# Kernel tuning notes

Hardware: AMD Instinct MI355X
Metric: run time of the kernel (lower is better)

The kernel has to match this reference:

```python
import jax, jax.numpy as jnp
import numpy as np

BLOCK_SIZE = 32
MODEL_DIM = 64
HEAD_SIZE = 64
WINDOW_SIZE = 8
B = 32768


def _local_causal_mask(T, window):
    # True = masked out. Allowed iff i - window + 1 <= j <= i.
    i = jnp.arange(T)[:, None]
    j = jnp.arange(T)[None, :]
    return (j > i) | (j < i - window + 1)


def setup_inputs() -> dict:
    key = jax.random.key(0)
    kx, kq, kk, kv = jax.random.split(key, 4)
    x = jax.random.normal(kx, (B, BLOCK_SIZE, MODEL_DIM), dtype=jnp.float32)
    # nn.Linear(model_dim, head_size, bias=False): y = x @ W.T, W: [head_size, model_dim].
    # Store as [model_dim, head_size] so y = x @ W.
    s = 1.0 / np.sqrt(MODEL_DIM)
    Wq = jax.random.uniform(kq, (MODEL_DIM, HEAD_SIZE), jnp.float32, -s, s)
    Wk = jax.random.uniform(kk, (MODEL_DIM, HEAD_SIZE), jnp.float32, -s, s)
    Wv = jax.random.uniform(kv, (MODEL_DIM, HEAD_SIZE), jnp.float32, -s, s)
    return {"x": x, "Wq": Wq, "Wk": Wk, "Wv": Wv}


def reference(x, Wq, Wk, Wv):
    B_, T, C = x.shape
    q = x @ Wq  # [B, T, H]
    k = x @ Wk
    v = x @ Wv
    scale = k.shape[-1] ** -0.5
    weight = jnp.einsum("bth,bsh->bts", q, k) * scale  # [B, T, T]
    mask = _local_causal_mask(T, WINDOW_SIZE)
    weight = jnp.where(mask[None, :, :], -jnp.inf, weight)
    attention_weights = jax.nn.softmax(weight, axis=-1)
    # dropout treated as identity (eval mode) for determinism
    output = jnp.einsum("bts,bsh->bth", attention_weights, v)
    return (output, attention_weights)
```

## Files before the change

### kernel.cpp

```cpp
#include <hip/hip_runtime.h>
#include <math.h>

typedef float f32x4 __attribute__((ext_vector_type(4)));
typedef unsigned int u32x4 __attribute__((ext_vector_type(4)));
typedef short bf16x8 __attribute__((ext_vector_type(8)));

__device__ __forceinline__ unsigned f2bf1(float f) {
  unsigned u = __builtin_bit_cast(unsigned, f);
  return (u + 0x7FFFu + ((u >> 16) & 1u)) >> 16;
}
__device__ __forceinline__ unsigned pack2(float a, float b) {
  return f2bf1(a) | (f2bf1(b) << 16);
}

__device__ __forceinline__ f32x4 mfma16(u32x4 a, u32x4 b, f32x4 c) {
  return __builtin_amdgcn_mfma_f32_16x16x32_bf16(
      __builtin_bit_cast(bf16x8, a), __builtin_bit_cast(bf16x8, b), c, 0, 0, 0);
}

template <int NS, int NF, int NKS>
__device__ __forceinline__ void cvt_frags(const f32x4 (&acc)[NS][NF],
                                          u32x4 (&frag)[NF][NKS],
                                          int f, int g) {
  unsigned pk[NS][NF][2];
#pragma unroll
  for (int s = 0; s < NS; ++s)
#pragma unroll
    for (int n = 0; n < NF; ++n) {
      pk[s][n][0] = pack2(acc[s][n][0], acc[s][n][1]);
      pk[s][n][1] = pack2(acc[s][n][2], acc[s][n][3]);
    }
  const bool hi = ((g >> 1) & 1) != 0;
#pragma unroll
  for (int w = 0; w < 4; ++w) {
    const int gp = 2 * (g & 1) + (w >> 1);
    const int idx = (f + (gp << 4)) << 2;
#pragma unroll
    for (int n = 0; n < NF; ++n)
#pragma unroll
      for (int ks = 0; ks < NKS; ++ks) {
        int lo = __builtin_amdgcn_ds_bpermute(idx, (int)pk[2 * ks + 0][n][w & 1]);
        int h2 = __builtin_amdgcn_ds_bpermute(idx, (int)pk[2 * ks + 1][n][w & 1]);
        frag[n][ks][w] = (unsigned)(hi ? h2 : lo);
      }
  }
}

__launch_bounds__(256, 2)
__global__ void lwmh_kernel(const float* __restrict__ x,
                            const float* __restrict__ Wq,
                            const float* __restrict__ Wk,
                            const float* __restrict__ Wv,
                            float* __restrict__ out,
                            float* __restrict__ attw,
                            int nb) {
  const int lane = threadIdx.x & 63;
  const int f = lane & 15;
  const int g = lane >> 4;
  const int wid = blockIdx.x * (blockDim.x >> 6) + (threadIdx.x >> 6);
  const int nwaves = gridDim.x * (blockDim.x >> 6);

  u32x4 aWq[4][2], bWkT[4][2];
#pragma unroll
  for (int ct = 0; ct < 4; ++ct)
#pragma unroll
    for (int hs = 0; hs < 2; ++hs) {
      const int off = (ct * 16 + f) * 64 + hs * 32 + g * 8;
      f32x4 ql = *(const f32x4*)(Wq + off);
      f32x4 qh = *(const f32x4*)(Wq + off + 4);
      f32x4 kl = *(const f32x4*)(Wk + off);
      f32x4 kh = *(const f32x4*)(Wk + off + 4);
      u32x4 fq, fk;
      fq[0] = pack2(ql[0], ql[1]); fq[1] = pack2(ql[2], ql[3]);
      fq[2] = pack2(qh[0], qh[1]); fq[3] = pack2(qh[2], qh[3]);
      fk[0] = pack2(kl[0], kl[1]); fk[1] = pack2(kl[2], kl[3]);
      fk[2] = pack2(kh[0], kh[1]); fk[3] = pack2(kh[2], kh[3]);
      aWq[ct][hs] = fq;
      bWkT[ct][hs] = fk;
    }

  u32x4 wv[4][2];
#pragma unroll
  for (int t = 0; t < 4; ++t)
#pragma unroll
    for (int ks = 0; ks < 2; ++ks) {
      const float* bv = Wv + (ks * 32 + g * 8) * 64 + t * 16 + f;
      u32x4 fv;
#pragma unroll
      for (int w = 0; w < 4; ++w)
        fv[w] = pack2(bv[(2 * w) * 64], bv[(2 * w + 1) * 64]);
      wv[t][ks] = fv;
    }

  u32x4 aN[4][2];
#pragma unroll
  for (int nc = 0; nc < 4; ++nc) {
    f32x4 nacc[4][1];
#pragma unroll
    for (int mc = 0; mc < 4; ++mc) {
      f32x4 a = {0.f, 0.f, 0.f, 0.f};
#pragma unroll
      for (int hs = 0; hs < 2; ++hs) a = mfma16(aWq[mc][hs], bWkT[nc][hs], a);
      nacc[mc][0] = a * 0.125f;
    }
    u32x4 tmp[1][2];
    cvt_frags<4, 1, 2>(nacc, tmp, f, g);
    aN[nc][0] = tmp[0][0];
    aN[nc][1] = tmp[0][1];
  }

  f32x4 xc[2][2][2], xn[2][2][2];

  auto loadX = [&](int b, f32x4 (&xr)[2][2][2]) {
    const float* xb = x + (size_t)b * 2048;
#pragma unroll
    for (int mt = 0; mt < 2; ++mt)
#pragma unroll
      for (int ks = 0; ks < 2; ++ks) {
        const float* p0 = xb + (mt * 16 + f) * 64 + ks * 32 + g * 8;
        xr[mt][ks][0] = *(const f32x4*)p0;
        xr[mt][ks][1] = *(const f32x4*)(p0 + 4);
      }
  };

  int b = wid;
  if (b < nb) loadX(b, xc);

  for (; b < nb; b += nwaves) {
    const int bn = b + nwaves;
    if (bn < nb) loadX(bn, xn);

    u32x4 xf[2][2];
#pragma unroll
    for (int mt = 0; mt < 2; ++mt)
#pragma unroll
      for (int ks = 0; ks < 2; ++ks) {
        u32x4 fr;
        fr[0] = pack2(xc[mt][ks][0][0], xc[mt][ks][0][1]);
        fr[1] = pack2(xc[mt][ks][0][2], xc[mt][ks][0][3]);
        fr[2] = pack2(xc[mt][ks][1][0], xc[mt][ks][1][1]);
        fr[3] = pack2(xc[mt][ks][1][2], xc[mt][ks][1][3]);
        xf[mt][ks] = fr;
      }

    f32x4 t2[4][2];
#pragma unroll
    for (int mc = 0; mc < 4; ++mc)
#pragma unroll
      for (int nt = 0; nt < 2; ++nt) {
        f32x4 a = {0.f, 0.f, 0.f, 0.f};
#pragma unroll
        for (int ks = 0; ks < 2; ++ks) a = mfma16(aN[mc][ks], xf[nt][ks], a);
        t2[mc][nt] = a;
      }
    u32x4 bT2[2][2];
    cvt_frags<4, 2, 2>(t2, bT2, f, g);

    f32x4 va[2][4];
#pragma unroll
    for (int ms = 0; ms < 2; ++ms)
#pragma unroll
      for (int nh = 0; nh < 4; ++nh) {
        f32x4 a = {0.f, 0.f, 0.f, 0.f};
#pragma unroll
        for (int ks = 0; ks < 2; ++ks) a = mfma16(xf[ms][ks], wv[nh][ks], a);
        va[ms][nh] = a;
      }
    u32x4 bV[4][1];
    cvt_frags<2, 4, 1>(va, bV, f, g);

    f32x4 st[2][2];
#pragma unroll
    for (int ms = 0; ms < 2; ++ms)
#pragma unroll
      for (int nt = 0; nt < 2; ++nt) {
        f32x4 a = {0.f, 0.f, 0.f, 0.f};
#pragma unroll
        for (int ks = 0; ks < 2; ++ks) a = mfma16(xf[ms][ks], bT2[nt][ks], a);
        st[ms][nt] = a;
      }

    f32x4 pe[2][2];
#pragma unroll
    for (int nt = 0; nt < 2; ++nt) {
      const int t = nt * 16 + f;
      float sum = 0.f;
#pragma unroll
      for (int ms = 0; ms < 2; ++ms)
#pragma unroll
        for (int r = 0; r < 4; ++r) {
          const int s = ms * 16 + 4 * g + r;
          const float e =
              ((unsigned)(t - s) <= 7u) ? __expf(st[ms][nt][r]) : 0.f;
          pe[ms][nt][r] = e;
          sum += e;
        }
      sum += __shfl_xor(sum, 16);
      sum += __shfl_xor(sum, 32);
      const float inv = 1.0f / sum;
#pragma unroll
      for (int ms = 0; ms < 2; ++ms)
        pe[ms][nt] *= inv;
    }

    {
      float* aw = attw + (size_t)b * 1024;
#pragma unroll
      for (int ms = 0; ms < 2; ++ms)
#pragma unroll
        for (int nt = 0; nt < 2; ++nt)
          *(f32x4*)(aw + (nt * 16 + f) * 32 + ms * 16 + 4 * g) = pe[ms][nt];
    }

    u32x4 aP[2][1];
    cvt_frags<2, 2, 1>(pe, aP, f, g);

    f32x4 o[2][4];
#pragma unroll
    for (int mt = 0; mt < 2; ++mt)
#pragma unroll
      for (int nh = 0; nh < 4; ++nh) {
        f32x4 a = {0.f, 0.f, 0.f, 0.f};
        o[mt][nh] = mfma16(aP[mt][0], bV[nh][0], a);
      }

    {
      float* op = out + (size_t)b * 2048;
#pragma unroll
      for (int mt = 0; mt < 2; ++mt)
#pragma unroll
        for (int nh = 0; nh < 4; ++nh)
#pragma unroll
          for (int r = 0; r < 4; ++r)
            op[(mt * 16 + 4 * g + r) * 64 + nh * 16 + f] = o[mt][nh][r];
    }

    if (bn < nb) {
#pragma unroll
      for (int mt = 0; mt < 2; ++mt)
#pragma unroll
        for (int ks = 0; ks < 2; ++ks) {
          xc[mt][ks][0] = xn[mt][ks][0];
          xc[mt][ks][1] = xn[mt][ks][1];
        }
    }
  }
}

extern "C" void kernel_launch(void* const* d_in, const int* in_sizes, int n_in,
                              void* d_out, int out_size, void* d_ws, size_t ws_size,
                              hipStream_t stream) {
  const float* x = (const float*)d_in[0];
  const float* Wq = (const float*)d_in[1];
  const float* Wk = (const float*)d_in[2];
  const float* Wv = (const float*)d_in[3];
  const int nb = in_sizes[0] / 2048;
  float* out = (float*)d_out;
  float* attw = out + (size_t)nb * 2048;

  const int grid = 1024;
  lwmh_kernel<<<grid, 256, 0, stream>>>(x, Wq, Wk, Wv, out, attw, nb);
}
```

Baseline: 146.3 us.

## Drop register prefetch of x, raise occupancy, use nontemporal loads/stores

Removes the software double-buffering of the next batch's x tile in registers, which frees registers so launch bounds can ask for 3 blocks per SM instead of 2. The grid shrinks from 1024 to 768 blocks. Global loads of x and stores of the outputs and attention weights become nontemporal to avoid polluting cache with streaming data. Latency hiding now depends on wave-level occupancy rather than explicit prefetch, which risks exposed load latency if occupancy doesn't actually rise.

```diff
diff --git a/kernel.cpp b/kernel.cpp
--- a/kernel.cpp
+++ b/kernel.cpp
@@ -46,7 +46,7 @@
   }
 }
 
-__launch_bounds__(256, 2)
+__launch_bounds__(256, 3)
 __global__ void lwmh_kernel(const float* __restrict__ x,
                             const float* __restrict__ Wq,
                             const float* __restrict__ Wk,
@@ -109,39 +109,25 @@
     aN[nc][1] = tmp[0][1];
   }
 
-  f32x4 xc[2][2][2], xn[2][2][2];
-
-  auto loadX = [&](int b, f32x4 (&xr)[2][2][2]) {
+  for (int b = wid; b < nb; b += nwaves) {
     const float* xb = x + (size_t)b * 2048;
-#pragma unroll
-    for (int mt = 0; mt < 2; ++mt)
-#pragma unroll
-      for (int ks = 0; ks < 2; ++ks) {
-        const float* p0 = xb + (mt * 16 + f) * 64 + ks * 32 + g * 8;
-        xr[mt][ks][0] = *(const f32x4*)p0;
-        xr[mt][ks][1] = *(const f32x4*)(p0 + 4);
-      }
-  };
-
-  int b = wid;
-  if (b < nb) loadX(b, xc);
-
-  for (; b < nb; b += nwaves) {
-    const int bn = b + nwaves;
-    if (bn < nb) loadX(bn, xn);
 
     u32x4 xf[2][2];
 #pragma unroll
-    for (int mt = 0; mt < 2; ++mt)
-#pragma unroll
-      for (int ks = 0; ks < 2; ++ks) {
-        u32x4 fr;
-        fr[0] = pack2(xc[mt][ks][0][0], xc[mt][ks][0][1]);
-        fr[1] = pack2(xc[mt][ks][0][2], xc[mt][ks][0][3]);
-        fr[2] = pack2(xc[mt][ks][1][0], xc[mt][ks][1][1]);
-        fr[3] = pack2(xc[mt][ks][1][2], xc[mt][ks][1][3]);
-        xf[mt][ks] = fr;
-      }
+    for (int mt = 0; mt < 2; ++mt) {
+      const float* p0 = xb + (mt * 16 + f) * 64 + g * 8;
+      f32x4 l00 = __builtin_nontemporal_load((const f32x4*)p0);
+      f32x4 l01 = __builtin_nontemporal_load((const f32x4*)(p0 + 4));
+      f32x4 l10 = __builtin_nontemporal_load((const f32x4*)(p0 + 32));
+      f32x4 l11 = __builtin_nontemporal_load((const f32x4*)(p0 + 36));
+      u32x4 fr0, fr1;
+      fr0[0] = pack2(l00[0], l00[1]); fr0[1] = pack2(l00[2], l00[3]);
+      fr0[2] = pack2(l01[0], l01[1]); fr0[3] = pack2(l01[2], l01[3]);
+      fr1[0] = pack2(l10[0], l10[1]); fr1[1] = pack2(l10[2], l10[3]);
+      fr1[2] = pack2(l11[0], l11[1]); fr1[3] = pack2(l11[2], l11[3]);
+      xf[mt][0] = fr0;
+      xf[mt][1] = fr1;
+    }
 
     f32x4 t2[4][2];
 #pragma unroll
@@ -209,7 +195,8 @@
       for (int ms = 0; ms < 2; ++ms)
 #pragma unroll
         for (int nt = 0; nt < 2; ++nt)
-          *(f32x4*)(aw + (nt * 16 + f) * 32 + ms * 16 + 4 * g) = pe[ms][nt];
+          __builtin_nontemporal_store(pe[ms][nt],
+              (f32x4*)(aw + (nt * 16 + f) * 32 + ms * 16 + 4 * g));
     }
 
     u32x4 aP[2][1];
@@ -232,17 +219,8 @@
         for (int nh = 0; nh < 4; ++nh)
 #pragma unroll
           for (int r = 0; r < 4; ++r)
-            op[(mt * 16 + 4 * g + r) * 64 + nh * 16 + f] = o[mt][nh][r];
-    }
-
-    if (bn < nb) {
-#pragma unroll
-      for (int mt = 0; mt < 2; ++mt)
-#pragma unroll
-        for (int ks = 0; ks < 2; ++ks) {
-          xc[mt][ks][0] = xn[mt][ks][0];
-          xc[mt][ks][1] = xn[mt][ks][1];
-        }
+            __builtin_nontemporal_store(o[mt][nh][r],
+                op + (mt * 16 + 4 * g + r) * 64 + nh * 16 + f);
     }
   }
 }
@@ -258,6 +236,6 @@
   float* out = (float*)d_out;
   float* attw = out + (size_t)nb * 2048;
 
-  const int grid = 1024;
+  const int grid = 768;
   lwmh_kernel<<<grid, 256, 0, stream>>>(x, Wq, Wk, Wv, out, attw, nb);
 }
```

New measurement: 164.4 us. +12.4%, slower.
